# Optimization experiments

Measured on AMD Instinct MI355X. Metric: run time of the kernel, lower is better.

Reference implementation:

```python
import jax, jax.numpy as jnp
import numpy as np

N_NODES = 256
COND = 64
ARCH = [256, 512, 1024]
E = N_NODES * (N_NODES - 1) // 2  # 32640 upper-triangular edges
OUT = 2 * E                        # 65280 final-layer width
B = 512
CUTOFF = 0.0
TAU = 1.0


def _make_params(key, dims):
    ws, bs = [], []
    for i, (din, dout) in enumerate(zip(dims[:-1], dims[1:])):
        k = jax.random.fold_in(key, i)
        kw, kb = jax.random.split(k)
        ws.append(jax.random.normal(kw, (din, dout), jnp.float32) * 0.02)
        bs.append(jax.random.normal(kb, (dout,), jnp.float32) * 0.02)
    return ws, bs


def setup_inputs() -> dict:
    key = jax.random.key(0)
    kx, kg, kbig, ksmall = jax.random.split(key, 4)
    x = jax.random.normal(kx, (B, COND), jnp.float32)
    gumbel = jax.random.gumbel(kg, (B, E, 2), jnp.float32)
    dims = [COND] + ARCH + [OUT]
    bw, bb = _make_params(kbig, dims)
    sw, sb = _make_params(ksmall, dims)
    inp = {"x": x, "gumbel": gumbel}
    for i in range(4):
        inp[f"bw{i}"] = bw[i]; inp[f"bb{i}"] = bb[i]
        inp[f"sw{i}"] = sw[i]; inp[f"sb{i}"] = sb[i]
    return inp


def _expert_adj(x, ws, bs, gumbel):
    # MLP: relu on all but last layer
    h = x
    for w, b in zip(ws[:-1], bs[:-1]):
        h = jax.nn.relu(h @ w + b)
    logits = (h @ ws[-1] + bs[-1]).reshape(x.shape[0], E, 2)
    # hard gumbel-softmax (straight-through), tau=1
    g = (logits + gumbel) / TAU
    y_soft = jax.nn.softmax(g, axis=-1)
    y_hard = jax.nn.one_hot(jnp.argmax(g, axis=-1), 2, dtype=y_soft.dtype)
    y = y_hard + y_soft - jax.lax.stop_gradient(y_soft)
    x0 = y[:, :, 0]  # [B, E]
    iu, ju = jnp.triu_indices(N_NODES, k=1)
    adj = jnp.zeros((x.shape[0], N_NODES, N_NODES), x0.dtype)
    adj = adj.at[:, iu, ju].set(x0)
    return adj + jnp.swapaxes(adj, 1, 2)


def reference(x, gumbel,
              bw0, bb0, bw1, bb1, bw2, bb2, bw3, bb3,
              sw0, sb0, sw1, sb1, sw2, sb2, sw3, sb3):
    big_ws, big_bs = [bw0, bw1, bw2, bw3], [bb0, bb1, bb2, bb3]
    small_ws, small_bs = [sw0, sw1, sw2, sw3], [sb0, sb1, sb2, sb3]
    adj_big = _expert_adj(x, big_ws, big_bs, gumbel)
    adj_small = _expert_adj(x, small_ws, small_bs, gumbel)
    mask_big = x[:, 0] > CUTOFF  # [B]
    out = jnp.where(mask_big[:, None, None], adj_big, adj_small)
    return out
```

## Files before the change

### kernel.cpp

```cpp
#include <hip/hip_runtime.h>

#define N_NODES 256
#define COND    64
#define E_PAIRS 32640
#define OUTCOLS 65280
#define BATCH   512
#define SLOTS   576
#define D1      256
#define D2      512
#define D3      1024

typedef __attribute__((ext_vector_type(8))) short bf16x8;
typedef __attribute__((ext_vector_type(4))) float f32x4;
typedef __attribute__((ext_vector_type(4))) unsigned int u32x4;

static __device__ __forceinline__ unsigned short f2bf(float f) {
    unsigned int u = __float_as_uint(f);
    u += 0x7FFF + ((u >> 16) & 1);
    return (unsigned short)(u >> 16);
}
static __device__ __forceinline__ float bf2f(unsigned short h) {
    return __uint_as_float(((unsigned int)h) << 16);
}

__global__ void k0_sort(const float* __restrict__ x, int* __restrict__ meta,
                        int* __restrict__ borig) {
    __shared__ int wc[9];
    int t = threadIdx.x;
    if (t < SLOTS) borig[t] = -1;
    int m = 0;
    if (t < BATCH) m = (x[t * COND] > 0.0f) ? 1 : 0;
    unsigned long long bm = __ballot(m);
    int wave = t >> 6;
    int lane = t & 63;
    int lanePre = __popcll(bm & ((1ull << lane) - 1ull));
    if (lane == 0) wc[wave] = __popcll(bm);
    __syncthreads();
    int nbig = 0, preBig = 0;
    #pragma unroll
    for (int w = 0; w < 8; ++w) {
        int c = wc[w];
        if (w < wave) preBig += c;
        nbig += c;
    }
    int S = (nbig + 63) & ~63;
    if (t < BATCH) {
        int onesBefore = preBig + lanePre;
        int slot = m ? onesBefore : (S + (t - onesBefore));
        borig[slot] = t;
    }
    if (t == 0) meta[0] = S;
}

template <bool GATHER, int K, int DOUT, bool SPLIT>
__global__ __launch_bounds__(256) void k1_gemm(
    const float* __restrict__ in,
    const float* __restrict__ wbig, const float* __restrict__ bbig,
    const float* __restrict__ wsml, const float* __restrict__ bsml,
    const int* __restrict__ meta, const int* __restrict__ borig,
    float* __restrict__ out, unsigned short* __restrict__ hbA) {
    __shared__ float hs[16][64 + 4];
    __shared__ float wt[16][64 + 4];
    int tid = threadIdx.x;
    int by = blockIdx.x;
    int bx = blockIdx.y;
    int r0 = by * 64;
    int cb = bx * 64;
    int S = meta[0];
    bool big = (r0 < S);
    const float* w = big ? wbig : wsml;
    const float* bias = big ? bbig : bsml;

    int lm = tid >> 2;
    int lq = tid & 3;
    int wk = tid >> 4;
    int wc = (tid & 15) * 4;

    int tm = tid >> 4;
    int tn = tid & 15;

    const float* hrow;
    if (GATHER) {
        int b = borig[r0 + lm];
        hrow = (b >= 0) ? &in[(size_t)b * K] : (const float*)0;
    } else {
        hrow = &in[(size_t)(r0 + lm) * K];
    }

    float acc[4][4];
    #pragma unroll
    for (int i = 0; i < 4; ++i)
        #pragma unroll
        for (int j = 0; j < 4; ++j) acc[i][j] = 0.f;

    for (int k0 = 0; k0 < K; k0 += 16) {
        float4 hv = make_float4(0.f, 0.f, 0.f, 0.f);
        if (!GATHER || hrow) hv = *(const float4*)&hrow[k0 + lq * 4];
        float4 wv = *(const float4*)&w[(size_t)(k0 + wk) * DOUT + cb + wc];
        __syncthreads();
        hs[lq * 4 + 0][lm] = hv.x;
        hs[lq * 4 + 1][lm] = hv.y;
        hs[lq * 4 + 2][lm] = hv.z;
        hs[lq * 4 + 3][lm] = hv.w;
        *(float4*)&wt[wk][wc] = wv;
        __syncthreads();
        #pragma unroll
        for (int kk = 0; kk < 16; ++kk) {
            float4 a  = *(const float4*)&hs[kk][tm * 4];
            float4 bf = *(const float4*)&wt[kk][tn * 4];
            acc[0][0] = fmaf(a.x, bf.x, acc[0][0]);
            acc[0][1] = fmaf(a.x, bf.y, acc[0][1]);
            acc[0][2] = fmaf(a.x, bf.z, acc[0][2]);
            acc[0][3] = fmaf(a.x, bf.w, acc[0][3]);
            acc[1][0] = fmaf(a.y, bf.x, acc[1][0]);
            acc[1][1] = fmaf(a.y, bf.y, acc[1][1]);
            acc[1][2] = fmaf(a.y, bf.z, acc[1][2]);
            acc[1][3] = fmaf(a.y, bf.w, acc[1][3]);
            acc[2][0] = fmaf(a.z, bf.x, acc[2][0]);
            acc[2][1] = fmaf(a.z, bf.y, acc[2][1]);
            acc[2][2] = fmaf(a.z, bf.z, acc[2][2]);
            acc[2][3] = fmaf(a.z, bf.w, acc[2][3]);
            acc[3][0] = fmaf(a.w, bf.x, acc[3][0]);
            acc[3][1] = fmaf(a.w, bf.y, acc[3][1]);
            acc[3][2] = fmaf(a.w, bf.z, acc[3][2]);
            acc[3][3] = fmaf(a.w, bf.w, acc[3][3]);
        }
    }

    float4 bv = *(const float4*)&bias[cb + tn * 4];
    #pragma unroll
    for (int i = 0; i < 4; ++i) {
        float o[4];
        o[0] = fmaxf(acc[i][0] + bv.x, 0.f);
        o[1] = fmaxf(acc[i][1] + bv.y, 0.f);
        o[2] = fmaxf(acc[i][2] + bv.z, 0.f);
        o[3] = fmaxf(acc[i][3] + bv.w, 0.f);
        if (SPLIT) {
            int row = r0 + tm * 4 + i;
            int by_ = row >> 6, rl = row & 63;
            int mfr = rl >> 4, p15 = rl & 15;
            int kt  = cb + tn * 4;
            int kk  = kt >> 5, lgk = (kt >> 3) & 3, j0 = kt & 7;
            size_t base = (size_t)(by_ * 32 + kk) * 6144 + (size_t)mfr * 512
                        + (size_t)(lgk * 16 + p15) * 8 + j0;
            ushort4 s0, s1, s2;
            unsigned short* q0[4] = {&s0.x, &s0.y, &s0.z, &s0.w};
            unsigned short* q1[4] = {&s1.x, &s1.y, &s1.z, &s1.w};
            unsigned short* q2[4] = {&s2.x, &s2.y, &s2.z, &s2.w};
            #pragma unroll
            for (int j = 0; j < 4; ++j) {
                unsigned short a0 = f2bf(o[j]);
                float r1v = o[j] - bf2f(a0);
                unsigned short a1 = f2bf(r1v);
                float r2v = r1v - bf2f(a1);
                *q0[j] = a0; *q1[j] = a1; *q2[j] = f2bf(r2v);
            }
            *(ushort4*)&hbA[base]        = s0;
            *(ushort4*)&hbA[base + 2048] = s1;
            *(ushort4*)&hbA[base + 4096] = s2;
        } else {
            float4 ov;
            ov.x = o[0]; ov.y = o[1]; ov.z = o[2]; ov.w = o[3];
            *(float4*)&out[(size_t)(r0 + tm * 4 + i) * DOUT + cb + tn * 4] = ov;
        }
    }
}

__global__ __launch_bounds__(256, 2) void k2_mfma(
    const unsigned short* __restrict__ hbA,
    const float* __restrict__ bw3, const float* __restrict__ bb3,
    const float* __restrict__ sw3, const float* __restrict__ sb3,
    const float* __restrict__ gum,
    const int* __restrict__ meta, const int* __restrict__ borig,
    unsigned char* __restrict__ bits) {
    int tid = threadIdx.x;
    int wgid = blockIdx.x;
    int xr  = wgid & 7;
    int s_  = wgid >> 3;
    int by  = s_ % 9;
    int q   = s_ / 9;
    int bx  = q * 8 + xr;
    if (bx >= 255) return;

    int r0 = by * 64;
    int db = bx * 128;
    int S = meta[0];
    bool big = (r0 < S);
    const float* w3 = big ? bw3 : sw3;
    const float* b3 = big ? bb3 : sb3;

    int lane = tid & 63;
    int wid  = tid >> 6;
    int l15  = lane & 15;
    int lg   = lane >> 4;

    int colg0 = db + wid * 32 + l15;

    f32x4 acc[4][2];
    #pragma unroll
    for (int m = 0; m < 4; ++m)
        #pragma unroll
        for (int n = 0; n < 2; ++n) acc[m][n] = (f32x4)0.f;

    const unsigned short* ap0 = hbA + (size_t)(by * 32) * 6144 + (size_t)lane * 8;
    const float* wbase = w3 + (size_t)(lg * 8) * OUTCOLS + 2 * (size_t)colg0;

#define LOADB(BUF, KK) do {                                                     \
    const float* wp_ = wbase + (size_t)(KK) * 32 * OUTCOLS;                     \
    _Pragma("unroll")                                                           \
    for (int n_ = 0; n_ < 2; ++n_) {                                            \
        _Pragma("unroll")                                                       \
        for (int j_ = 0; j_ < 8; ++j_)                                          \
            BUF[n_ * 8 + j_] = *(const float2*)(wp_ + (size_t)j_ * OUTCOLS      \
                                                + n_ * 32);                     \
    }                                                                           \
} while (0)

#define STEP(BUF, KK) do {                                                      \
    const unsigned short* ap_ = ap0 + (size_t)(KK) * 6144;                      \
    bf16x8 af_[3][4];                                                           \
    _Pragma("unroll")                                                           \
    for (int l_ = 0; l_ < 3; ++l_)                                              \
        _Pragma("unroll")                                                       \
        for (int m_ = 0; m_ < 4; ++m_)                                          \
            af_[l_][m_] = *(const bf16x8*)(ap_ + l_ * 2048 + m_ * 512);         \
    _Pragma("unroll")                                                           \
    for (int n_ = 0; n_ < 2; ++n_) {                                            \
        u32x4 f0_, f1_, f2_;                                                    \
        _Pragma("unroll")                                                       \
        for (int w_ = 0; w_ < 4; ++w_) {                                        \
            float dA_ = BUF[n_ * 8 + 2 * w_].x     - BUF[n_ * 8 + 2 * w_].y;    \
            float dB_ = BUF[n_ * 8 + 2 * w_ + 1].x - BUF[n_ * 8 + 2 * w_ + 1].y;\
            unsigned short aL_ = f2bf(dA_), aH_ = f2bf(dB_);                    \
            f0_[w_] = (unsigned int)aL_ | ((unsigned int)aH_ << 16);            \
            float rA_ = dA_ - bf2f(aL_), rB_ = dB_ - bf2f(aH_);                 \
            unsigned short bL_ = f2bf(rA_), bH_ = f2bf(rB_);                    \
            f1_[w_] = (unsigned int)bL_ | ((unsigned int)bH_ << 16);            \
            float sA_ = rA_ - bf2f(bL_), sB_ = rB_ - bf2f(bH_);                 \
            f2_[w_] = (unsigned int)f2bf(sA_) | ((unsigned int)f2bf(sB_) << 16);\
        }                                                                       \
        bf16x8 b0_ = __builtin_bit_cast(bf16x8, f0_);                           \
        bf16x8 b1_ = __builtin_bit_cast(bf16x8, f1_);                           \
        bf16x8 b2_ = __builtin_bit_cast(bf16x8, f2_);                           \
        _Pragma("unroll")                                                       \
        for (int m_ = 0; m_ < 4; ++m_) {                                        \
            f32x4 c_ = acc[m_][n_];                                             \
            c_ = __builtin_amdgcn_mfma_f32_16x16x32_bf16(af_[0][m_], b0_, c_, 0, 0, 0); \
            c_ = __builtin_amdgcn_mfma_f32_16x16x32_bf16(af_[0][m_], b1_, c_, 0, 0, 0); \
            c_ = __builtin_amdgcn_mfma_f32_16x16x32_bf16(af_[1][m_], b0_, c_, 0, 0, 0); \
            c_ = __builtin_amdgcn_mfma_f32_16x16x32_bf16(af_[1][m_], b1_, c_, 0, 0, 0); \
            c_ = __builtin_amdgcn_mfma_f32_16x16x32_bf16(af_[0][m_], b2_, c_, 0, 0, 0); \
            c_ = __builtin_amdgcn_mfma_f32_16x16x32_bf16(af_[2][m_], b0_, c_, 0, 0, 0); \
            acc[m_][n_] = c_;                                                   \
        }                                                                       \
    }                                                                           \
} while (0)

    float2 brE[16], brO[16];
    LOADB(brE, 0);
    asm volatile("" ::: "memory");
    for (int ki = 0; ki < 16; ++ki) {
        int ke = ki * 2;
        LOADB(brO, ke + 1);
        asm volatile("" ::: "memory");
        STEP(brE, ke);
        LOADB(brE, (ki < 15) ? ke + 2 : 31);
        asm volatile("" ::: "memory");
        STEP(brO, ke + 1);
    }
#undef LOADB
#undef STEP

    #pragma unroll
    for (int n = 0; n < 2; ++n) {
        int colg = db + wid * 32 + n * 16 + l15;
        float2 bv = *(const float2*)&b3[2 * colg];
        float bd = bv.x - bv.y;
        #pragma unroll
        for (int m = 0; m < 4; ++m) {
            #pragma unroll
            for (int r = 0; r < 4; ++r) {
                int slot = r0 + m * 16 + lg * 4 + r;
                int b = borig[slot];
                if (b < 0) continue;
                float2 gv = *(const float2*)&gum[(size_t)b * OUTCOLS + 2 * colg];
                float g = acc[m][n][r] + bd + (gv.x - gv.y);
                bits[(size_t)b * E_PAIRS + colg] = (g >= 0.f) ? 1 : 0;
            }
        }
    }
}

__global__ __launch_bounds__(256) void k3_expand(
    const unsigned char* __restrict__ bits, float* __restrict__ out) {
    __shared__ unsigned char L[64][68];
    int p = blockIdx.x;
    int ti = (p >= 4) + (p >= 7) + (p >= 9);
    int off = (ti == 0) ? 0 : (ti == 1) ? 4 : (ti == 2) ? 7 : 9;
    int tj = ti + (p - off);
    int b = blockIdx.y;
    int t = threadIdx.x;

    {
        int r = t >> 2;
        int q = t & 3;
        int i = ti * 64 + r;
        long base = (long)b * E_PAIRS + (long)i * (511 - i) / 2 - i - 1;
        int j0 = tj * 64 + q * 16;
        #pragma unroll
        for (int k = 0; k < 16; ++k) {
            int j = j0 + k;
            unsigned char v = (j > i) ? bits[base + j] : (unsigned char)0;
            L[r][q * 16 + k] = v;
        }
    }
    __syncthreads();

    int h  = t >> 4;
    int w4 = (t & 15) * 4;

    {
        #pragma unroll
        for (int rr = 0; rr < 4; ++rr) {
            int ii = rr * 16 + h;
            int i_ = ti * 64 + ii;
            float4 v;
            if (ti == tj) {
                int jj;
                jj = w4 + 0; v.x = (jj > ii) ? (float)L[ii][jj] : (jj < ii ? (float)L[jj][ii] : 0.f);
                jj = w4 + 1; v.y = (jj > ii) ? (float)L[ii][jj] : (jj < ii ? (float)L[jj][ii] : 0.f);
                jj = w4 + 2; v.z = (jj > ii) ? (float)L[ii][jj] : (jj < ii ? (float)L[jj][ii] : 0.f);
                jj = w4 + 3; v.w = (jj > ii) ? (float)L[ii][jj] : (jj < ii ? (float)L[jj][ii] : 0.f);
            } else {
                v.x = (float)L[ii][w4 + 0];
                v.y = (float)L[ii][w4 + 1];
                v.z = (float)L[ii][w4 + 2];
                v.w = (float)L[ii][w4 + 3];
            }
            size_t o = (((size_t)b * 256 + i_) * 256) + tj * 64 + w4;
            *(float4*)&out[o] = v;
        }
    }

    if (ti != tj) {
        #pragma unroll
        for (int rr = 0; rr < 4; ++rr) {
            int jj = rr * 16 + h;
            int j_ = tj * 64 + jj;
            float4 v;
            v.x = (float)L[w4 + 0][jj];
            v.y = (float)L[w4 + 1][jj];
            v.z = (float)L[w4 + 2][jj];
            v.w = (float)L[w4 + 3][jj];
            size_t o = (((size_t)b * 256 + j_) * 256) + ti * 64 + w4;
            *(float4*)&out[o] = v;
        }
    }
}

extern "C" void kernel_launch(void* const* d_in, const int* in_sizes, int n_in,
                              void* d_out, int out_size, void* d_ws, size_t ws_size,
                              hipStream_t stream) {
    const float* x   = (const float*)d_in[0];
    const float* gum = (const float*)d_in[1];
    const float* bw0 = (const float*)d_in[2];  const float* bb0 = (const float*)d_in[3];
    const float* sw0 = (const float*)d_in[4];  const float* sb0 = (const float*)d_in[5];
    const float* bw1 = (const float*)d_in[6];  const float* bb1 = (const float*)d_in[7];
    const float* sw1 = (const float*)d_in[8];  const float* sb1 = (const float*)d_in[9];
    const float* bw2 = (const float*)d_in[10]; const float* bb2 = (const float*)d_in[11];
    const float* sw2 = (const float*)d_in[12]; const float* sb2 = (const float*)d_in[13];
    const float* bw3 = (const float*)d_in[14]; const float* bb3 = (const float*)d_in[15];
    const float* sw3 = (const float*)d_in[16]; const float* sb3 = (const float*)d_in[17];

    char* ws = (char*)d_ws;
    int*   meta  = (int*)ws;
    int*   borig = (int*)(ws + 64);
    float* act1  = (float*)(ws + 4096);
    float* act2  = (float*)(ws + 593920);
    unsigned short* hbA = (unsigned short*)(ws + 1773568);
    unsigned char* bits = (unsigned char*)(ws + 5312512);
    float* out = (float*)d_out;

    k0_sort<<<1, SLOTS, 0, stream>>>(x, meta, borig);
    k1_gemm<true,  COND, D1, false><<<dim3(9, D1 / 64), 256, 0, stream>>>(
        x,    bw0, bb0, sw0, sb0, meta, borig, act1, 0);
    k1_gemm<false, D1,   D2, false><<<dim3(9, D2 / 64), 256, 0, stream>>>(
        act1, bw1, bb1, sw1, sb1, meta, borig, act2, 0);
    k1_gemm<false, D2,   D3, true><<<dim3(9, D3 / 64), 256, 0, stream>>>(
        act2, bw2, bb2, sw2, sb2, meta, borig, (float*)0, hbA);
    k2_mfma<<<2304, 256, 0, stream>>>(hbA, bw3, bb3, sw3, sb3, gum,
                                      meta, borig, bits);
    k3_expand<<<dim3(10, BATCH), 256, 0, stream>>>(bits, out);
}
```

Before: 1.028 ms.

## Pre-split final-layer weights into packed bf16x3 column chunks before MFMA GEMM

Adds a prepass kernel that converts the final-layer fp32 weight differences into three packed bf16 residual planes laid out for direct MFMA B-operand loads. The main GEMM is split into big and small expert phases over two column halves, and each phase reads the pre-packed planes instead of converting strided fp32 loads inside the inner loop. This removes per-tile conversion work and uncoalesced weight reads, at the cost of extra kernel launches, an extra write and read of the split buffer, and a larger workspace requirement. The old fused kernel is kept as a fallback when the workspace is too small.

```diff
diff --git a/kernel.cpp b/kernel.cpp
--- a/kernel.cpp
+++ b/kernel.cpp
@@ -9,6 +9,9 @@
 #define D1      256
 #define D2      512
 #define D3      1024
+#define COLCAP  16384
+#define LSTRU   (COLCAP * 16)
+#define TSTRU   (3 * COLCAP * 16)
 
 typedef __attribute__((ext_vector_type(8))) short bf16x8;
 typedef __attribute__((ext_vector_type(4))) float f32x4;
@@ -166,7 +169,128 @@
     }
 }
 
-__global__ __launch_bounds__(256, 2) void k2_mfma(
+__global__ __launch_bounds__(256) void kp_split(
+    const float* __restrict__ w3, unsigned int* __restrict__ bb,
+    int colsBase, int ncols) {
+    int tid = threadIdx.x;
+    int cx = blockIdx.x;
+    int t  = blockIdx.y;
+    int c  = cx * 256 + tid;
+    if (c >= ncols) return;
+    const float* wp = w3 + (size_t)(t * 32) * OUTCOLS + 2 * (size_t)(colsBase + c);
+    unsigned int L0[16], L1[16], L2[16];
+    #pragma unroll
+    for (int kk = 0; kk < 32; kk += 2) {
+        float2 a = *(const float2*)(wp + (size_t)kk * OUTCOLS);
+        float2 b = *(const float2*)(wp + (size_t)(kk + 1) * OUTCOLS);
+        float dA = a.x - a.y, dB = b.x - b.y;
+        unsigned short aL = f2bf(dA), aH = f2bf(dB);
+        L0[kk >> 1] = (unsigned)aL | ((unsigned)aH << 16);
+        float rA = dA - bf2f(aL), rB = dB - bf2f(aH);
+        unsigned short bL = f2bf(rA), bH = f2bf(rB);
+        L1[kk >> 1] = (unsigned)bL | ((unsigned)bH << 16);
+        float sA = rA - bf2f(bL), sB = rB - bf2f(bH);
+        L2[kk >> 1] = (unsigned)f2bf(sA) | ((unsigned)f2bf(sB) << 16);
+    }
+    unsigned int* p = bb + (size_t)t * TSTRU + (size_t)c * 16;
+    #pragma unroll
+    for (int i = 0; i < 4; ++i) {
+        u32x4 v0 = {L0[4*i], L0[4*i+1], L0[4*i+2], L0[4*i+3]};
+        u32x4 v1 = {L1[4*i], L1[4*i+1], L1[4*i+2], L1[4*i+3]};
+        u32x4 v2 = {L2[4*i], L2[4*i+1], L2[4*i+2], L2[4*i+3]};
+        *(u32x4*)(p + i * 4)             = v0;
+        *(u32x4*)(p + LSTRU + i * 4)     = v1;
+        *(u32x4*)(p + 2 * LSTRU + i * 4) = v2;
+    }
+}
+
+template <bool BIGPHASE>
+__global__ __launch_bounds__(256) void k2p(
+    const unsigned short* __restrict__ hbA, const unsigned int* __restrict__ bb,
+    const float* __restrict__ bb3, const float* __restrict__ sb3,
+    const float* __restrict__ gum, const int* __restrict__ meta,
+    const int* __restrict__ borig, unsigned char* __restrict__ bits,
+    int ctBase, int ntiles) {
+    int tid = threadIdx.x;
+    int wgid = blockIdx.x;
+    int xr = wgid & 7;
+    int s_ = wgid >> 3;
+    int unit = xr * 144 + s_;
+    if (unit >= 9 * ntiles) return;
+    int ct = unit / 9;
+    int by = unit % 9;
+    int S = meta[0];
+    bool big = (by * 64 < S);
+    if (big != BIGPHASE) return;
+    int r0 = by * 64;
+
+    int lane = tid & 63;
+    int wid  = tid >> 6;
+    int l15  = lane & 15;
+    int lg   = lane >> 4;
+
+    int lc    = ct * 128 + wid * 32 + l15;
+    int colg0 = ctBase * 128 + lc;
+
+    f32x4 acc[4][2];
+    #pragma unroll
+    for (int m = 0; m < 4; ++m)
+        #pragma unroll
+        for (int n = 0; n < 2; ++n) acc[m][n] = (f32x4)0.f;
+
+    const unsigned short* ap0 = hbA + (size_t)(by * 32) * 6144 + (size_t)lane * 8;
+    const unsigned int*   bp0 = bb + (size_t)lc * 16 + lg * 4;
+
+    for (int t = 0; t < 32; ++t) {
+        const unsigned short* ap = ap0 + (size_t)t * 6144;
+        bf16x8 af[3][4];
+        #pragma unroll
+        for (int l = 0; l < 3; ++l)
+            #pragma unroll
+            for (int m = 0; m < 4; ++m)
+                af[l][m] = *(const bf16x8*)(ap + l * 2048 + m * 512);
+        const unsigned int* bp = bp0 + (size_t)t * TSTRU;
+        #pragma unroll
+        for (int n = 0; n < 2; ++n) {
+            bf16x8 b0 = __builtin_bit_cast(bf16x8, *(const u32x4*)(bp + n * 256));
+            bf16x8 b1 = __builtin_bit_cast(bf16x8, *(const u32x4*)(bp + LSTRU + n * 256));
+            bf16x8 b2 = __builtin_bit_cast(bf16x8, *(const u32x4*)(bp + 2 * LSTRU + n * 256));
+            #pragma unroll
+            for (int m = 0; m < 4; ++m) {
+                f32x4 c = acc[m][n];
+                c = __builtin_amdgcn_mfma_f32_16x16x32_bf16(af[0][m], b0, c, 0, 0, 0);
+                c = __builtin_amdgcn_mfma_f32_16x16x32_bf16(af[0][m], b1, c, 0, 0, 0);
+                c = __builtin_amdgcn_mfma_f32_16x16x32_bf16(af[1][m], b0, c, 0, 0, 0);
+                c = __builtin_amdgcn_mfma_f32_16x16x32_bf16(af[1][m], b1, c, 0, 0, 0);
+                c = __builtin_amdgcn_mfma_f32_16x16x32_bf16(af[0][m], b2, c, 0, 0, 0);
+                c = __builtin_amdgcn_mfma_f32_16x16x32_bf16(af[2][m], b0, c, 0, 0, 0);
+                acc[m][n] = c;
+            }
+        }
+    }
+
+    const float* b3 = BIGPHASE ? bb3 : sb3;
+    #pragma unroll
+    for (int n = 0; n < 2; ++n) {
+        int colg = colg0 + n * 16;
+        float2 bv = *(const float2*)&b3[2 * colg];
+        float bd = bv.x - bv.y;
+        #pragma unroll
+        for (int m = 0; m < 4; ++m) {
+            #pragma unroll
+            for (int r = 0; r < 4; ++r) {
+                int slot = r0 + m * 16 + lg * 4 + r;
+                int b = borig[slot];
+                if (b < 0) continue;
+                float2 gv = *(const float2*)&gum[(size_t)b * OUTCOLS + 2 * colg];
+                float g = acc[m][n][r] + bd + (gv.x - gv.y);
+                bits[(size_t)b * E_PAIRS + colg] = (g >= 0.f) ? 1 : 0;
+            }
+        }
+    }
+}
+
+__global__ __launch_bounds__(256, 3) void k2_fb(
     const unsigned short* __restrict__ hbA,
     const float* __restrict__ bw3, const float* __restrict__ bb3,
     const float* __restrict__ sw3, const float* __restrict__ sb3,
@@ -193,7 +317,6 @@
     int wid  = tid >> 6;
     int l15  = lane & 15;
     int lg   = lane >> 4;
-
     int colg0 = db + wid * 32 + l15;
 
     f32x4 acc[4][2];
@@ -258,14 +381,11 @@
 
     float2 brE[16], brO[16];
     LOADB(brE, 0);
-    asm volatile("" ::: "memory");
     for (int ki = 0; ki < 16; ++ki) {
         int ke = ki * 2;
         LOADB(brO, ke + 1);
-        asm volatile("" ::: "memory");
         STEP(brE, ke);
         LOADB(brE, (ki < 15) ? ke + 2 : 31);
-        asm volatile("" ::: "memory");
         STEP(brO, ke + 1);
     }
 #undef LOADB
@@ -379,7 +499,11 @@
     float* act2  = (float*)(ws + 593920);
     unsigned short* hbA = (unsigned short*)(ws + 1773568);
     unsigned char* bits = (unsigned char*)(ws + 5312512);
+    unsigned int* bb = (unsigned int*)(ws + 22024192);
     float* out = (float*)d_out;
+
+    size_t need_pre = 22024192ull + (size_t)32 * TSTRU * 4;
+    bool pre = (ws_size >= need_pre);
 
     k0_sort<<<1, SLOTS, 0, stream>>>(x, meta, borig);
     k1_gemm<true,  COND, D1, false><<<dim3(9, D1 / 64), 256, 0, stream>>>(
@@ -388,7 +512,19 @@
         act1, bw1, bb1, sw1, sb1, meta, borig, act2, 0);
     k1_gemm<false, D2,   D3, true><<<dim3(9, D3 / 64), 256, 0, stream>>>(
         act2, bw2, bb2, sw2, sb2, meta, borig, (float*)0, hbA);
-    k2_mfma<<<2304, 256, 0, stream>>>(hbA, bw3, bb3, sw3, sb3, gum,
-                                      meta, borig, bits);
+
+    if (pre) {
+        kp_split<<<dim3(64, 32), 256, 0, stream>>>(bw3, bb, 0, 16384);
+        k2p<true ><<<1152, 256, 0, stream>>>(hbA, bb, bb3, sb3, gum, meta, borig, bits, 0, 128);
+        kp_split<<<dim3(64, 32), 256, 0, stream>>>(sw3, bb, 0, 16384);
+        k2p<false><<<1152, 256, 0, stream>>>(hbA, bb, bb3, sb3, gum, meta, borig, bits, 0, 128);
+        kp_split<<<dim3(64, 32), 256, 0, stream>>>(bw3, bb, 16384, 16256);
+        k2p<true ><<<1152, 256, 0, stream>>>(hbA, bb, bb3, sb3, gum, meta, borig, bits, 128, 127);
+        kp_split<<<dim3(64, 32), 256, 0, stream>>>(sw3, bb, 16384, 16256);
+        k2p<false><<<1152, 256, 0, stream>>>(hbA, bb, bb3, sb3, gum, meta, borig, bits, 128, 127);
+    } else {
+        k2_fb<<<2304, 256, 0, stream>>>(hbA, bw3, bb3, sw3, sb3, gum,
+                                        meta, borig, bits);
+    }
     k3_expand<<<dim3(10, BATCH), 256, 0, stream>>>(bits, out);
 }
```

Measured after the change: 1.225 ms. +19.1%, slower.

## Split final-layer GEMM between MFMA and FP32 SIMT paths by workgroup parity

Applied to the files above, without the earlier changes.

The final-layer kernel becomes a hybrid. Even column groups keep the bf16x3-split MFMA path, while odd groups run an FP32 FMA tiled GEMM on the fp32 activations. That tiled path precomputes logit differences (w0-w1), so it needs only half the output columns. The third GEMM now also writes fp32 activations to a new buffer, and the MFMA-side compiler memory barriers were removed. The aim is to run matrix and vector units concurrently and halve the FLOPs on the SIMT path, at the cost of extra activation writes and uneven per-workgroup work.

```diff
diff --git a/kernel.cpp b/kernel.cpp
--- a/kernel.cpp
+++ b/kernel.cpp
@@ -135,6 +135,9 @@
         o[1] = fmaxf(acc[i][1] + bv.y, 0.f);
         o[2] = fmaxf(acc[i][2] + bv.z, 0.f);
         o[3] = fmaxf(acc[i][3] + bv.w, 0.f);
+        float4 ov;
+        ov.x = o[0]; ov.y = o[1]; ov.z = o[2]; ov.w = o[3];
+        *(float4*)&out[(size_t)(r0 + tm * 4 + i) * DOUT + cb + tn * 4] = ov;
         if (SPLIT) {
             int row = r0 + tm * 4 + i;
             int by_ = row >> 6, rl = row & 63;
@@ -158,52 +161,55 @@
             *(ushort4*)&hbA[base]        = s0;
             *(ushort4*)&hbA[base + 2048] = s1;
             *(ushort4*)&hbA[base + 4096] = s2;
-        } else {
-            float4 ov;
-            ov.x = o[0]; ov.y = o[1]; ov.z = o[2]; ov.w = o[3];
-            *(float4*)&out[(size_t)(r0 + tm * 4 + i) * DOUT + cb + tn * 4] = ov;
-        }
-    }
-}
-
-__global__ __launch_bounds__(256, 2) void k2_mfma(
-    const unsigned short* __restrict__ hbA,
+        }
+    }
+}
+
+#define BM   64
+#define BNW  256
+#define BND  128
+#define BK   16
+__global__ __launch_bounds__(256, 4) void k2_hybrid(
+    const float* __restrict__ hbuf, const unsigned short* __restrict__ hbA,
     const float* __restrict__ bw3, const float* __restrict__ bb3,
     const float* __restrict__ sw3, const float* __restrict__ sb3,
     const float* __restrict__ gum,
     const int* __restrict__ meta, const int* __restrict__ borig,
     unsigned char* __restrict__ bits) {
+    __shared__ float hs[BK][BM + 4];
+    __shared__ float wt[BK][BND + 4];
+
     int tid = threadIdx.x;
     int wgid = blockIdx.x;
     int xr  = wgid & 7;
     int s_  = wgid >> 3;
     int by  = s_ % 9;
     int q   = s_ / 9;
-    int bx  = q * 8 + xr;
-    if (bx >= 255) return;
+    int ct  = q * 8 + xr;
+    if (ct >= 255) return;
 
     int r0 = by * 64;
-    int db = bx * 128;
     int S = meta[0];
     bool big = (r0 < S);
     const float* w3 = big ? bw3 : sw3;
     const float* b3 = big ? bb3 : sb3;
 
-    int lane = tid & 63;
-    int wid  = tid >> 6;
-    int l15  = lane & 15;
-    int lg   = lane >> 4;
-
-    int colg0 = db + wid * 32 + l15;
-
-    f32x4 acc[4][2];
-    #pragma unroll
-    for (int m = 0; m < 4; ++m)
-        #pragma unroll
-        for (int n = 0; n < 2; ++n) acc[m][n] = (f32x4)0.f;
-
-    const unsigned short* ap0 = hbA + (size_t)(by * 32) * 6144 + (size_t)lane * 8;
-    const float* wbase = w3 + (size_t)(lg * 8) * OUTCOLS + 2 * (size_t)colg0;
+    if ((q & 1) == 0) {
+        int lane = tid & 63;
+        int wid  = tid >> 6;
+        int l15  = lane & 15;
+        int lg   = lane >> 4;
+        int db   = ct * 128;
+        int colg0 = db + wid * 32 + l15;
+
+        f32x4 acc[4][2];
+        #pragma unroll
+        for (int m = 0; m < 4; ++m)
+            #pragma unroll
+            for (int n = 0; n < 2; ++n) acc[m][n] = (f32x4)0.f;
+
+        const unsigned short* ap0 = hbA + (size_t)(by * 32) * 6144 + (size_t)lane * 8;
+        const float* wbase = w3 + (size_t)(lg * 8) * OUTCOLS + 2 * (size_t)colg0;
 
 #define LOADB(BUF, KK) do {                                                     \
     const float* wp_ = wbase + (size_t)(KK) * 32 * OUTCOLS;                     \
@@ -256,37 +262,110 @@
     }                                                                           \
 } while (0)
 
-    float2 brE[16], brO[16];
-    LOADB(brE, 0);
-    asm volatile("" ::: "memory");
-    for (int ki = 0; ki < 16; ++ki) {
-        int ke = ki * 2;
-        LOADB(brO, ke + 1);
-        asm volatile("" ::: "memory");
-        STEP(brE, ke);
-        LOADB(brE, (ki < 15) ? ke + 2 : 31);
-        asm volatile("" ::: "memory");
-        STEP(brO, ke + 1);
-    }
+        float2 brE[16], brO[16];
+        LOADB(brE, 0);
+        for (int ki = 0; ki < 16; ++ki) {
+            int ke = ki * 2;
+            LOADB(brO, ke + 1);
+            STEP(brE, ke);
+            LOADB(brE, (ki < 15) ? ke + 2 : 31);
+            STEP(brO, ke + 1);
+        }
 #undef LOADB
 #undef STEP
 
-    #pragma unroll
-    for (int n = 0; n < 2; ++n) {
-        int colg = db + wid * 32 + n * 16 + l15;
-        float2 bv = *(const float2*)&b3[2 * colg];
-        float bd = bv.x - bv.y;
-        #pragma unroll
-        for (int m = 0; m < 4; ++m) {
+        #pragma unroll
+        for (int n = 0; n < 2; ++n) {
+            int colg = db + wid * 32 + n * 16 + l15;
+            float2 bv = *(const float2*)&b3[2 * colg];
+            float bd = bv.x - bv.y;
             #pragma unroll
-            for (int r = 0; r < 4; ++r) {
-                int slot = r0 + m * 16 + lg * 4 + r;
-                int b = borig[slot];
-                if (b < 0) continue;
-                float2 gv = *(const float2*)&gum[(size_t)b * OUTCOLS + 2 * colg];
-                float g = acc[m][n][r] + bd + (gv.x - gv.y);
-                bits[(size_t)b * E_PAIRS + colg] = (g >= 0.f) ? 1 : 0;
+            for (int m = 0; m < 4; ++m) {
+                #pragma unroll
+                for (int r = 0; r < 4; ++r) {
+                    int slot = r0 + m * 16 + lg * 4 + r;
+                    int b = borig[slot];
+                    if (b < 0) continue;
+                    float2 gv = *(const float2*)&gum[(size_t)b * OUTCOLS + 2 * colg];
+                    float g = acc[m][n][r] + bd + (gv.x - gv.y);
+                    bits[(size_t)b * E_PAIRS + colg] = (g >= 0.f) ? 1 : 0;
+                }
             }
+        }
+    } else {
+        int cb = ct * BNW;
+
+        int lm  = tid >> 2;
+        int lq  = tid & 3;
+        int wk  = tid >> 4;
+        int wcc = (tid & 15) * 16;
+        int wd  = (tid & 15) * 8;
+
+        int tm = tid >> 5;
+        int tn = tid & 31;
+
+        float acc[8][4];
+        #pragma unroll
+        for (int i = 0; i < 8; ++i)
+            #pragma unroll
+            for (int j = 0; j < 4; ++j) acc[i][j] = 0.f;
+
+        for (int k0 = 0; k0 < D3; k0 += BK) {
+            float4 hv = *(const float4*)&hbuf[(size_t)(r0 + lm) * D3 + k0 + lq * 4];
+            const float* wrow = &w3[(size_t)(k0 + wk) * OUTCOLS + cb + wcc];
+            float4 wv0 = *(const float4*)&wrow[0];
+            float4 wv1 = *(const float4*)&wrow[4];
+            float4 wv2 = *(const float4*)&wrow[8];
+            float4 wv3 = *(const float4*)&wrow[12];
+            __syncthreads();
+            hs[lq * 4 + 0][lm] = hv.x;
+            hs[lq * 4 + 1][lm] = hv.y;
+            hs[lq * 4 + 2][lm] = hv.z;
+            hs[lq * 4 + 3][lm] = hv.w;
+            float4 d0, d1;
+            d0.x = wv0.x - wv0.y;  d0.y = wv0.z - wv0.w;
+            d0.z = wv1.x - wv1.y;  d0.w = wv1.z - wv1.w;
+            d1.x = wv2.x - wv2.y;  d1.y = wv2.z - wv2.w;
+            d1.z = wv3.x - wv3.y;  d1.w = wv3.z - wv3.w;
+            *(float4*)&wt[wk][wd]     = d0;
+            *(float4*)&wt[wk][wd + 4] = d1;
+            __syncthreads();
+            #pragma unroll
+            for (int kk = 0; kk < BK; ++kk) {
+                float4 a0 = *(const float4*)&hs[kk][tm * 8];
+                float4 a1 = *(const float4*)&hs[kk][tm * 8 + 4];
+                float4 bf = *(const float4*)&wt[kk][tn * 4];
+                float am[8] = {a0.x, a0.y, a0.z, a0.w, a1.x, a1.y, a1.z, a1.w};
+                float bn[4] = {bf.x, bf.y, bf.z, bf.w};
+                #pragma unroll
+                for (int i = 0; i < 8; ++i)
+                    #pragma unroll
+                    for (int j = 0; j < 4; ++j)
+                        acc[i][j] = fmaf(am[i], bn[j], acc[i][j]);
+            }
+        }
+
+        float4 bv0 = *(const float4*)&b3[cb + tn * 8];
+        float4 bv1 = *(const float4*)&b3[cb + tn * 8 + 4];
+        float bd0 = bv0.x - bv0.y;
+        float bd1 = bv0.z - bv0.w;
+        float bd2 = bv1.x - bv1.y;
+        float bd3 = bv1.z - bv1.w;
+        int ebase = ct * BND + tn * 4;
+        #pragma unroll
+        for (int i = 0; i < 8; ++i) {
+            int slot = r0 + tm * 8 + i;
+            int b = borig[slot];
+            if (b < 0) continue;
+            const float* gp = &gum[(size_t)b * OUTCOLS + (size_t)ebase * 2];
+            float4 gv0 = *(const float4*)&gp[0];
+            float4 gv1 = *(const float4*)&gp[4];
+            uchar4 v;
+            v.x = ((acc[i][0] + bd0) + (gv0.x - gv0.y) >= 0.f) ? 1 : 0;
+            v.y = ((acc[i][1] + bd1) + (gv0.z - gv0.w) >= 0.f) ? 1 : 0;
+            v.z = ((acc[i][2] + bd2) + (gv1.x - gv1.y) >= 0.f) ? 1 : 0;
+            v.w = ((acc[i][3] + bd3) + (gv1.z - gv1.w) >= 0.f) ? 1 : 0;
+            *(uchar4*)&bits[(size_t)b * E_PAIRS + ebase] = v;
         }
     }
 }
@@ -377,8 +456,9 @@
     int*   borig = (int*)(ws + 64);
     float* act1  = (float*)(ws + 4096);
     float* act2  = (float*)(ws + 593920);
-    unsigned short* hbA = (unsigned short*)(ws + 1773568);
-    unsigned char* bits = (unsigned char*)(ws + 5312512);
+    float* hbuf  = (float*)(ws + 1773568);
+    unsigned short* hbA = (unsigned short*)(ws + 4132864);
+    unsigned char* bits = (unsigned char*)(ws + 7671808);
     float* out = (float*)d_out;
 
     k0_sort<<<1, SLOTS, 0, stream>>>(x, meta, borig);
@@ -387,8 +467,8 @@
     k1_gemm<false, D1,   D2, false><<<dim3(9, D2 / 64), 256, 0, stream>>>(
         act1, bw1, bb1, sw1, sb1, meta, borig, act2, 0);
     k1_gemm<false, D2,   D3, true><<<dim3(9, D3 / 64), 256, 0, stream>>>(
-        act2, bw2, bb2, sw2, sb2, meta, borig, (float*)0, hbA);
-    k2_mfma<<<2304, 256, 0, stream>>>(hbA, bw3, bb3, sw3, sb3, gum,
-                                      meta, borig, bits);
+        act2, bw2, bb2, sw2, sb2, meta, borig, hbuf, hbA);
+    k2_hybrid<<<2304, 256, 0, stream>>>(hbuf, hbA, bw3, bb3, sw3, sb3, gum,
+                                        meta, borig, bits);
     k3_expand<<<dim3(10, BATCH), 256, 0, stream>>>(bits, out);
 }
```

Result: slower. 1.132 ms (+10.0%).
